# Kernel optimization log

Hardware: AMD Instinct MI355X
Metric: run time of the kernel (lower is better)

## Reference

```python
import jax, jax.numpy as jnp
import numpy as np

N = 20000        # nodes
E = 640000       # edges (avg degree 32)
D_IN = 128       # node_features
D_HID = 256      # conv_booster * D_IN
D_DENSE = 128    # D_HID // linear_decay
N_CLASSES = 2


def _glorot(key, fan_in, fan_out):
    s = np.sqrt(1.0 / fan_in).astype(np.float32)
    return jax.random.normal(key, (fan_in, fan_out), jnp.float32) * s


def setup_inputs() -> dict:
    key = jax.random.key(0)
    ks = jax.random.split(key, 12)
    return {
        "node_features": jax.random.normal(ks[0], (N, D_IN), jnp.float32),
        "edge_index": jax.random.randint(ks[1], (2, E), 0, N, dtype=jnp.int32),
        "edge_weight": jax.random.uniform(ks[2], (E,), jnp.float32),
        "W1": _glorot(ks[3], D_IN, D_HID),
        "b1": jnp.zeros((D_HID,), jnp.float32),
        "W2": _glorot(ks[4], D_HID, D_HID),
        "b2": jnp.zeros((D_HID,), jnp.float32),
        "Wd1": _glorot(ks[5], D_HID, D_DENSE),
        "bd1": jnp.zeros((D_DENSE,), jnp.float32),
        "Wd2": _glorot(ks[6], D_DENSE, N_CLASSES),
        "bd2": jnp.zeros((N_CLASSES,), jnp.float32),
    }


def gcn_conv(x, row, col, w, W, b, n):
    # PyG GCNConv: add self-loops (weight 1), symmetric normalization,
    # x' = D^{-1/2}(A+I)D^{-1/2} (x W) + b
    h = x @ W                                        # [n, out]
    loop = jnp.arange(n, dtype=row.dtype)
    r = jnp.concatenate([row, loop])
    c = jnp.concatenate([col, loop])
    ww = jnp.concatenate([w, jnp.ones((n,), w.dtype)])
    deg = jax.ops.segment_sum(ww, c, num_segments=n)  # degree at targets
    dinv = jnp.where(deg > 0, jax.lax.rsqrt(deg), 0.0)
    norm = dinv[r] * ww * dinv[c]                    # [E+n]
    msg = norm[:, None] * h[r]                       # gather + scale (hot path)
    return jax.ops.segment_sum(msg, c, num_segments=n) + b  # scatter-add


def reference(node_features, edge_index, edge_weight,
              W1, b1, W2, b2, Wd1, bd1, Wd2, bd2):
    row, col = edge_index[0], edge_index[1]
    n = node_features.shape[0]
    h = gcn_conv(node_features, row, col, edge_weight, W1, b1, n)
    h = gcn_conv(h, row, col, edge_weight, W2, b2, n)
    g = jnp.mean(h, axis=0)                          # MeanAggregation pooling
    z = jax.nn.relu(g @ Wd1 + bd1)
    logits = z @ Wd2 + bd2
    return jax.nn.softmax(logits)
```

## Files before the change

kernel.cpp:

```cpp
#include <hip/hip_runtime.h>
#include <hip/hip_bf16.h>


#define D_IN 128
#define D_HID 256
#define D_DENSE 128
#define R0 10240
#define NSL 128
#define NFOLD 250
#define FOLD_C 80
#define NTILE 157

__global__ __launch_bounds__(1024) void k_scatter(
    const int* __restrict__ tgt, const int* __restrict__ src,
    const float* __restrict__ w, const float* __restrict__ dinv,
    const float* __restrict__ u, float* __restrict__ part,
    unsigned* __restrict__ ctr, int E, int N, int mode) {
    __shared__ float acc[R0];
    if (mode == 0 && blockIdx.x == 0 && threadIdx.x == 0) ctr[0] = 0u;
    const int range = blockIdx.x & 1;
    const int slice = blockIdx.x >> 1;
    const int base  = range ? R0 : 0;
    const int lim   = range ? (N - R0) : R0;
    const int per = (E + NSL - 1) / NSL;
    const int e0 = slice * per, e1 = min(e0 + per, E);
    float* outp = part + (range ? (size_t)NSL * R0 + (size_t)slice * lim
                                : (size_t)slice * lim);
    for (int i = threadIdx.x; i < lim; i += 1024) acc[i] = 0.f;
    __syncthreads();
    for (int e = e0 + threadIdx.x; e < e1; e += 1024) {
        int t = tgt[e] - base;
        if ((unsigned)t < (unsigned)lim) {
            float v = w[e];
            if (mode != 0) {
                int c = src[e];
                float dc = dinv[c];
                v *= (mode == 2) ? dc * u[c] : dc;
            }
            atomicAdd(&acc[t], v);
        }
    }
    __syncthreads();
    for (int i = threadIdx.x; i < lim; i += 1024) outp[i] = acc[i];
}

__global__ __launch_bounds__(1024) void k_fold(
    const float* __restrict__ part, float* __restrict__ dinv,
    float* __restrict__ u, float* __restrict__ S_u_part,
    const float* __restrict__ W1, const float* __restrict__ b1,
    const float* __restrict__ W2, float* __restrict__ M, float* __restrict__ c2,
    int N, int mode) {
    __shared__ float lds[1044];
    const int b = blockIdx.x, tid = threadIdx.x;

    if (b >= NFOLD) {
        int q = b - NFOLD;
        lds[tid] = W2[(tid >> 2) * 256 + q * 4 + (tid & 3)];
        __syncthreads();
        int wvi = tid >> 6, lane = tid & 63;
        for (int kr = 0; kr < 8; ++kr) {
            int k = wvi * 8 + kr;
            float a0 = 0, a1 = 0, a2 = 0, a3 = 0;
            #pragma unroll
            for (int it = 0; it < 4; ++it) {
                int j = it * 64 + lane;
                float a = W1[k * 256 + j];
                a0 += a * lds[j*4+0]; a1 += a * lds[j*4+1];
                a2 += a * lds[j*4+2]; a3 += a * lds[j*4+3];
            }
            #pragma unroll
            for (int off = 32; off > 0; off >>= 1) {
                a0 += __shfl_down(a0, off, 64); a1 += __shfl_down(a1, off, 64);
                a2 += __shfl_down(a2, off, 64); a3 += __shfl_down(a3, off, 64);
            }
            if (lane == 0) {
                M[k * 256 + q*4 + 0] = a0; M[k * 256 + q*4 + 1] = a1;
                M[k * 256 + q*4 + 2] = a2; M[k * 256 + q*4 + 3] = a3;
            }
        }
        if (wvi == 0) {
            float a0 = 0, a1 = 0, a2 = 0, a3 = 0;
            #pragma unroll
            for (int it = 0; it < 4; ++it) {
                int j = it * 64 + lane;
                float a = b1[j];
                a0 += a * lds[j*4+0]; a1 += a * lds[j*4+1];
                a2 += a * lds[j*4+2]; a3 += a * lds[j*4+3];
            }
            #pragma unroll
            for (int off = 32; off > 0; off >>= 1) {
                a0 += __shfl_down(a0, off, 64); a1 += __shfl_down(a1, off, 64);
                a2 += __shfl_down(a2, off, 64); a3 += __shfl_down(a3, off, 64);
            }
            if (lane == 0) {
                c2[q*4+0] = a0; c2[q*4+1] = a1;
                c2[q*4+2] = a2; c2[q*4+3] = a3;
            }
        }
        return;
    }

    const int j = tid & 127, rg = tid >> 7;
    const int i = b * FOLD_C + j;
    const bool act = (j < FOLD_C) && (i < N);
    float sv = 0.f;
    if (act) {
        size_t st; const float* pp;
        if (i < R0) { st = R0;               pp = part + i; }
        else        { st = (size_t)(N - R0); pp = part + (size_t)NSL * R0 + (i - R0); }
        pp += (size_t)rg * 16 * st;
        #pragma unroll
        for (int r = 0; r < 16; ++r) sv += pp[(size_t)r * st];
    }
    lds[rg * 128 + j] = sv;
    __syncthreads();
    float ui = 0.f;
    if (rg == 0) {
        float tot = 0.f;
        #pragma unroll
        for (int q = 0; q < 8; ++q) tot += lds[q * 128 + j];
        if (act) {
            if (mode == 0) dinv[i] = rsqrtf(tot + 1.0f);
            else { float d = dinv[i]; ui = d * (tot + d); u[i] = ui; }
        }
    }
    if (mode == 1) {
        float v = ui;
        #pragma unroll
        for (int off = 32; off > 0; off >>= 1) v += __shfl_down(v, off, 64);
        if ((tid & 63) == 0) lds[1028 + (tid >> 6)] = v;
        __syncthreads();
        if (tid == 0) {
            float t2 = 0.f;
            #pragma unroll
            for (int q = 0; q < 16; ++q) t2 += lds[1028 + q];
            S_u_part[b] = t2;
        }
    }
}

__device__ __forceinline__ void g_arrive(unsigned* ctr) {
    __syncthreads();
    if (threadIdx.x == 0)
        __hip_atomic_fetch_add(ctr, 1u, __ATOMIC_RELEASE, __HIP_MEMORY_SCOPE_AGENT);
}
__device__ __forceinline__ void g_wait(unsigned* ctr, unsigned target) {
    if (threadIdx.x == 0) {
        while (__hip_atomic_load(ctr, __ATOMIC_ACQUIRE, __HIP_MEMORY_SCOPE_AGENT) < target)
            __builtin_amdgcn_s_sleep(2);
    }
    __syncthreads();
}

__global__ __launch_bounds__(1024) void k_tail(
    const float* __restrict__ x, const float* __restrict__ part,
    const float* __restrict__ dinv, const float* __restrict__ u,
    const float* __restrict__ S_u_part, const float* __restrict__ M,
    const float* __restrict__ c2, const float* __restrict__ b2,
    const float* __restrict__ Wd1, const float* __restrict__ bd1,
    const float* __restrict__ Wd2, const float* __restrict__ bd2,
    float* __restrict__ s_part, float* __restrict__ g_part,
    float* __restrict__ z_part, float* __restrict__ S_u_g,
    unsigned* __restrict__ ctr, float* __restrict__ out,
    int N, float inv_n) {
    __shared__ float sh[1024];
    __shared__ float wvl[128];
    __shared__ float ss[128];
    __shared__ float gv[16];
    __shared__ float su[16];
    const int b = blockIdx.x, tid = threadIdx.x;
    const int k = tid & 127, rg = tid >> 7;

    if (b < NTILE) {
        const int i0 = b * 128;
        const int i = i0 + k;
        const bool act = i < N;
        float sv = 0.f;
        if (act) {
            size_t st; const float* pp;
            if (i < R0) { st = R0;               pp = part + i; }
            else        { st = (size_t)(N - R0); pp = part + (size_t)NSL * R0 + (i - R0); }
            pp += (size_t)rg * 16 * st;
            #pragma unroll
            for (int r = 0; r < 16; ++r) sv += pp[(size_t)r * st];
        }
        sh[tid] = sv;
        __syncthreads();
        if (rg == 0) {
            float q = 0.f;
            #pragma unroll
            for (int t2 = 0; t2 < 8; ++t2) q += sh[t2 * 128 + k];
            float d = act ? dinv[i] : 0.f;
            wvl[k] = act ? d * (q + d * u[i]) : 0.f;
        }
        __syncthreads();
        float acc = 0.f;
        #pragma unroll
        for (int jj = 0; jj < 16; ++jj) {
            int m = rg + 8 * jj;
            int i2 = i0 + m;
            float xv = x[(size_t)(i2 < N ? i2 : i0) * D_IN + k];
            acc += wvl[m] * xv;
        }
        sh[tid] = acc;
        __syncthreads();
        if (rg == 0) {
            float t2s = 0.f;
            #pragma unroll
            for (int t2 = 0; t2 < 8; ++t2) t2s += sh[t2 * 128 + k];
            s_part[b * 128 + k] = t2s;
        }
    }
    g_arrive(ctr);
    if (b >= 16) return;
    g_wait(ctr, 256);

    {
        float a2 = 0.f;
        for (int q = rg; q < NTILE; q += 8) a2 += s_part[q * 128 + k];
        sh[tid] = a2;
        float v = 0.f;
        if (b == 0) {
            v = (tid < NFOLD) ? S_u_part[tid] : 0.f;
            #pragma unroll
            for (int off = 32; off > 0; off >>= 1) v += __shfl_down(v, off, 64);
        }
        __syncthreads();
        if (rg == 0) {
            float t2 = 0.f;
            #pragma unroll
            for (int q = 0; q < 8; ++q) t2 += sh[q * 128 + k];
            ss[k] = t2;
        }
        if (b == 0 && (tid & 63) == 0) su[tid >> 6] = v;
        __syncthreads();
        if (b == 0 && tid == 0) {
            float t2 = 0.f;
            #pragma unroll
            for (int q = 0; q < 16; ++q) t2 += su[q];
            S_u_g[0] = t2;
        }
        if (tid < 256) {
            float gp = 0.f;
            #pragma unroll
            for (int kk = 0; kk < 8; ++kk)
                gp += ss[b * 8 + kk] * M[(b * 8 + kk) * 256 + tid];
            g_part[b * 256 + tid] = gp;
        }
    }
    g_arrive(ctr);
    g_wait(ctr, 272);

    {
        if (tid < 16) {
            int kk = b * 16 + tid;
            float gval = 0.f;
            #pragma unroll
            for (int p2 = 0; p2 < 16; ++p2) gval += g_part[p2 * 256 + kk];
            gv[tid] = (gval + S_u_g[0] * c2[kk]) * inv_n + b2[kk];
        }
        __syncthreads();
        if (tid < 128) {
            float z = 0.f;
            #pragma unroll
            for (int kk = 0; kk < 16; ++kk)
                z += gv[kk] * Wd1[(b * 16 + kk) * D_DENSE + tid];
            z_part[b * 128 + tid] = z;
        }
    }
    g_arrive(ctr);
    if (b != 0) return;
    g_wait(ctr, 288);

    float p0 = 0.f, p1 = 0.f;
    if (tid < 128) {
        float zr = bd1[tid];
        #pragma unroll
        for (int p2 = 0; p2 < 16; ++p2) zr += z_part[p2 * 128 + tid];
        float zt = fmaxf(zr, 0.f);
        p0 = zt * Wd2[tid * 2 + 0];
        p1 = zt * Wd2[tid * 2 + 1];
    }
    #pragma unroll
    for (int off = 32; off > 0; off >>= 1) {
        p0 += __shfl_down(p0, off, 64);
        p1 += __shfl_down(p1, off, 64);
    }
    if ((tid & 63) == 0) { sh[tid >> 6] = p0; sh[32 + (tid >> 6)] = p1; }
    __syncthreads();
    if (tid == 0) {
        float l0 = bd2[0], l1 = bd2[1];
        #pragma unroll
        for (int q = 0; q < 16; ++q) { l0 += sh[q]; l1 += sh[32 + q]; }
        float m = fmaxf(l0, l1);
        float e0 = expf(l0 - m), e1 = expf(l1 - m);
        float inv = 1.0f / (e0 + e1);
        out[0] = e0 * inv;
        out[1] = e1 * inv;
    }
}

extern "C" void kernel_launch(void* const* d_in, const int* in_sizes, int n_in,
                              void* d_out, int out_size, void* d_ws, size_t ws_size,
                              hipStream_t stream) {
    const float* x   = (const float*)d_in[0];
    const int*   ei  = (const int*)  d_in[1];
    const float* w   = (const float*)d_in[2];
    const float* W1  = (const float*)d_in[3];
    const float* b1  = (const float*)d_in[4];
    const float* W2  = (const float*)d_in[5];
    const float* b2  = (const float*)d_in[6];
    const float* Wd1 = (const float*)d_in[7];
    const float* bd1 = (const float*)d_in[8];
    const float* Wd2 = (const float*)d_in[9];
    const float* bd2 = (const float*)d_in[10];
    float* out = (float*)d_out;

    const int N = in_sizes[0] / D_IN;
    const int E = in_sizes[1] / 2;
    const int* row = ei;
    const int* col = ei + E;

    unsigned* ctr = (unsigned*)d_ws;
    float* fws    = (float*)d_ws + 16;
    float* part   = fws;
    float* dinv   = part + (size_t)NSL * N;
    float* u      = dinv + N;
    float* s_part = u + N;
    float* S_u_p  = s_part + (size_t)NTILE * D_IN;
    float* S_u_g  = S_u_p + NFOLD;
    float* M      = S_u_g + 1;
    float* c2     = M + D_IN * D_HID;
    float* g_part = c2 + D_HID;
    float* z_part = g_part + 16 * D_HID;

    k_scatter<<<2 * NSL, 1024, 0, stream>>>(col, row, w, dinv, u, part, ctr, E, N, 0);
    k_fold<<<NFOLD + 64, 1024, 0, stream>>>(part, dinv, u, S_u_p, W1, b1, W2, M, c2, N, 0);
    k_scatter<<<2 * NSL, 1024, 0, stream>>>(row, col, w, dinv, u, part, ctr, E, N, 1);
    k_fold<<<NFOLD, 1024, 0, stream>>>(part, dinv, u, S_u_p, W1, b1, W2, M, c2, N, 1);
    k_scatter<<<2 * NSL, 1024, 0, stream>>>(row, col, w, dinv, u, part, ctr, E, N, 2);
    k_tail<<<256, 1024, 0, stream>>>(x, part, dinv, u, S_u_p, M, c2, b2,
                                     Wd1, bd1, Wd2, bd2, s_part, g_part, z_part,
                                     S_u_g, ctr, out, N, 1.0f / (float)N);
}
```

Before: 149.9 us.

## Fuse all stages into one persistent kernel with grid-wide barriers

Replaces the six separate launches (three scatters, two folds, tail) with a single 256-block persistent kernel. The stages are separated by atomic-counter grid barriers, and the counter is reset with a memset beforehand. The fold grid shrinks from 250 to 192 blocks so it fits inside the persistent grid, and the W1·W2 precompute moves onto the leftover blocks. The aim is to remove kernel launch gaps and inter-kernel drain. The cost is a spin-wait on every barrier, and the kernel relies on all 256 blocks being co-resident.

```diff
diff --git a/kernel.cpp b/kernel.cpp
--- a/kernel.cpp
+++ b/kernel.cpp
@@ -7,137 +7,9 @@
 #define D_DENSE 128
 #define R0 10240
 #define NSL 128
-#define NFOLD 250
-#define FOLD_C 80
+#define FOLD_B 192
+#define FOLD_C 105
 #define NTILE 157
-
-__global__ __launch_bounds__(1024) void k_scatter(
-    const int* __restrict__ tgt, const int* __restrict__ src,
-    const float* __restrict__ w, const float* __restrict__ dinv,
-    const float* __restrict__ u, float* __restrict__ part,
-    unsigned* __restrict__ ctr, int E, int N, int mode) {
-    __shared__ float acc[R0];
-    if (mode == 0 && blockIdx.x == 0 && threadIdx.x == 0) ctr[0] = 0u;
-    const int range = blockIdx.x & 1;
-    const int slice = blockIdx.x >> 1;
-    const int base  = range ? R0 : 0;
-    const int lim   = range ? (N - R0) : R0;
-    const int per = (E + NSL - 1) / NSL;
-    const int e0 = slice * per, e1 = min(e0 + per, E);
-    float* outp = part + (range ? (size_t)NSL * R0 + (size_t)slice * lim
-                                : (size_t)slice * lim);
-    for (int i = threadIdx.x; i < lim; i += 1024) acc[i] = 0.f;
-    __syncthreads();
-    for (int e = e0 + threadIdx.x; e < e1; e += 1024) {
-        int t = tgt[e] - base;
-        if ((unsigned)t < (unsigned)lim) {
-            float v = w[e];
-            if (mode != 0) {
-                int c = src[e];
-                float dc = dinv[c];
-                v *= (mode == 2) ? dc * u[c] : dc;
-            }
-            atomicAdd(&acc[t], v);
-        }
-    }
-    __syncthreads();
-    for (int i = threadIdx.x; i < lim; i += 1024) outp[i] = acc[i];
-}
-
-__global__ __launch_bounds__(1024) void k_fold(
-    const float* __restrict__ part, float* __restrict__ dinv,
-    float* __restrict__ u, float* __restrict__ S_u_part,
-    const float* __restrict__ W1, const float* __restrict__ b1,
-    const float* __restrict__ W2, float* __restrict__ M, float* __restrict__ c2,
-    int N, int mode) {
-    __shared__ float lds[1044];
-    const int b = blockIdx.x, tid = threadIdx.x;
-
-    if (b >= NFOLD) {
-        int q = b - NFOLD;
-        lds[tid] = W2[(tid >> 2) * 256 + q * 4 + (tid & 3)];
-        __syncthreads();
-        int wvi = tid >> 6, lane = tid & 63;
-        for (int kr = 0; kr < 8; ++kr) {
-            int k = wvi * 8 + kr;
-            float a0 = 0, a1 = 0, a2 = 0, a3 = 0;
-            #pragma unroll
-            for (int it = 0; it < 4; ++it) {
-                int j = it * 64 + lane;
-                float a = W1[k * 256 + j];
-                a0 += a * lds[j*4+0]; a1 += a * lds[j*4+1];
-                a2 += a * lds[j*4+2]; a3 += a * lds[j*4+3];
-            }
-            #pragma unroll
-            for (int off = 32; off > 0; off >>= 1) {
-                a0 += __shfl_down(a0, off, 64); a1 += __shfl_down(a1, off, 64);
-                a2 += __shfl_down(a2, off, 64); a3 += __shfl_down(a3, off, 64);
-            }
-            if (lane == 0) {
-                M[k * 256 + q*4 + 0] = a0; M[k * 256 + q*4 + 1] = a1;
-                M[k * 256 + q*4 + 2] = a2; M[k * 256 + q*4 + 3] = a3;
-            }
-        }
-        if (wvi == 0) {
-            float a0 = 0, a1 = 0, a2 = 0, a3 = 0;
-            #pragma unroll
-            for (int it = 0; it < 4; ++it) {
-                int j = it * 64 + lane;
-                float a = b1[j];
-                a0 += a * lds[j*4+0]; a1 += a * lds[j*4+1];
-                a2 += a * lds[j*4+2]; a3 += a * lds[j*4+3];
-            }
-            #pragma unroll
-            for (int off = 32; off > 0; off >>= 1) {
-                a0 += __shfl_down(a0, off, 64); a1 += __shfl_down(a1, off, 64);
-                a2 += __shfl_down(a2, off, 64); a3 += __shfl_down(a3, off, 64);
-            }
-            if (lane == 0) {
-                c2[q*4+0] = a0; c2[q*4+1] = a1;
-                c2[q*4+2] = a2; c2[q*4+3] = a3;
-            }
-        }
-        return;
-    }
-
-    const int j = tid & 127, rg = tid >> 7;
-    const int i = b * FOLD_C + j;
-    const bool act = (j < FOLD_C) && (i < N);
-    float sv = 0.f;
-    if (act) {
-        size_t st; const float* pp;
-        if (i < R0) { st = R0;               pp = part + i; }
-        else        { st = (size_t)(N - R0); pp = part + (size_t)NSL * R0 + (i - R0); }
-        pp += (size_t)rg * 16 * st;
-        #pragma unroll
-        for (int r = 0; r < 16; ++r) sv += pp[(size_t)r * st];
-    }
-    lds[rg * 128 + j] = sv;
-    __syncthreads();
-    float ui = 0.f;
-    if (rg == 0) {
-        float tot = 0.f;
-        #pragma unroll
-        for (int q = 0; q < 8; ++q) tot += lds[q * 128 + j];
-        if (act) {
-            if (mode == 0) dinv[i] = rsqrtf(tot + 1.0f);
-            else { float d = dinv[i]; ui = d * (tot + d); u[i] = ui; }
-        }
-    }
-    if (mode == 1) {
-        float v = ui;
-        #pragma unroll
-        for (int off = 32; off > 0; off >>= 1) v += __shfl_down(v, off, 64);
-        if ((tid & 63) == 0) lds[1028 + (tid >> 6)] = v;
-        __syncthreads();
-        if (tid == 0) {
-            float t2 = 0.f;
-            #pragma unroll
-            for (int q = 0; q < 16; ++q) t2 += lds[1028 + q];
-            S_u_part[b] = t2;
-        }
-    }
-}
 
 __device__ __forceinline__ void g_arrive(unsigned* ctr) {
     __syncthreads();
@@ -152,28 +24,132 @@
     __syncthreads();
 }
 
-__global__ __launch_bounds__(1024) void k_tail(
-    const float* __restrict__ x, const float* __restrict__ part,
-    const float* __restrict__ dinv, const float* __restrict__ u,
-    const float* __restrict__ S_u_part, const float* __restrict__ M,
-    const float* __restrict__ c2, const float* __restrict__ b2,
+__global__ __launch_bounds__(1024) void k_all(
+    const float* __restrict__ x, const int* __restrict__ row,
+    const int* __restrict__ col, const float* __restrict__ w,
+    const float* __restrict__ W1, const float* __restrict__ b1,
+    const float* __restrict__ W2, const float* __restrict__ b2,
     const float* __restrict__ Wd1, const float* __restrict__ bd1,
     const float* __restrict__ Wd2, const float* __restrict__ bd2,
-    float* __restrict__ s_part, float* __restrict__ g_part,
-    float* __restrict__ z_part, float* __restrict__ S_u_g,
+    float* __restrict__ part, float* __restrict__ dinv, float* __restrict__ u,
+    float* __restrict__ s_part, float* __restrict__ S_u_part,
+    float* __restrict__ S_u_g, float* __restrict__ M, float* __restrict__ c2,
+    float* __restrict__ g_part, float* __restrict__ z_part,
     unsigned* __restrict__ ctr, float* __restrict__ out,
-    int N, float inv_n) {
-    __shared__ float sh[1024];
-    __shared__ float wvl[128];
-    __shared__ float ss[128];
-    __shared__ float gv[16];
-    __shared__ float su[16];
+    int N, int E, float inv_n) {
+    __shared__ float lds[R0];
     const int b = blockIdx.x, tid = threadIdx.x;
-    const int k = tid & 127, rg = tid >> 7;
-
-    if (b < NTILE) {
-        const int i0 = b * 128;
-        const int i = i0 + k;
+
+    auto scatter = [&](const int* tgt, const int* src, int mode) {
+        const int range = b & 1, slice = b >> 1;
+        const int base = range ? R0 : 0;
+        const int lim  = range ? (N - R0) : R0;
+        const int per = (E + NSL - 1) / NSL;
+        const int e0 = slice * per, e1 = min(e0 + per, E);
+        float* outp = part + (range ? (size_t)NSL * R0 + (size_t)slice * lim
+                                    : (size_t)slice * lim);
+        for (int i = tid; i < lim; i += 1024) lds[i] = 0.f;
+        __syncthreads();
+        for (int e = e0 + tid; e < e1; e += 1024) {
+            int t = tgt[e] - base;
+            if ((unsigned)t < (unsigned)lim) {
+                float v = w[e];
+                if (mode != 0) {
+                    int c = src[e];
+                    float dc = dinv[c];
+                    v *= (mode == 2) ? dc * u[c] : dc;
+                }
+                atomicAdd(&lds[t], v);
+            }
+        }
+        __syncthreads();
+        for (int i = tid; i < lim; i += 1024) outp[i] = lds[i];
+    };
+
+    auto fold = [&](int mode) {
+        const int j = tid & 127, rg = tid >> 7;
+        const int i = b * FOLD_C + j;
+        const bool act = (j < FOLD_C) && (i < N);
+        float sv = 0.f;
+        if (act) {
+            size_t st; const float* pp;
+            if (i < R0) { st = R0;               pp = part + i; }
+            else        { st = (size_t)(N - R0); pp = part + (size_t)NSL * R0 + (i - R0); }
+            pp += (size_t)rg * 16 * st;
+            #pragma unroll
+            for (int r = 0; r < 16; ++r) sv += pp[(size_t)r * st];
+        }
+        lds[rg * 128 + j] = sv;
+        __syncthreads();
+        float ui = 0.f;
+        if (rg == 0) {
+            float tot = 0.f;
+            #pragma unroll
+            for (int q = 0; q < 8; ++q) tot += lds[q * 128 + j];
+            if (act) {
+                if (mode == 0) dinv[i] = rsqrtf(tot + 1.0f);
+                else { float d = dinv[i]; ui = d * (tot + d); u[i] = ui; }
+            }
+        }
+        if (mode == 1) {
+            float v = ui;
+            #pragma unroll
+            for (int off = 32; off > 0; off >>= 1) v += __shfl_down(v, off, 64);
+            if (tid < 128 && (tid & 63) == 0) lds[1030 + (tid >> 6)] = v;
+            __syncthreads();
+            if (tid == 0) S_u_part[b] = lds[1030] + lds[1031];
+        }
+    };
+
+    auto precompute = [&]() {
+        int q = b - FOLD_B;
+        lds[tid] = W2[(tid >> 2) * 256 + q * 4 + (tid & 3)];
+        __syncthreads();
+        int wvi = tid >> 6, lane = tid & 63;
+        for (int kr = 0; kr < 8; ++kr) {
+            int k = wvi * 8 + kr;
+            float a0 = 0, a1 = 0, a2 = 0, a3 = 0;
+            #pragma unroll
+            for (int it = 0; it < 4; ++it) {
+                int j = it * 64 + lane;
+                float a = W1[k * 256 + j];
+                a0 += a * lds[j*4+0]; a1 += a * lds[j*4+1];
+                a2 += a * lds[j*4+2]; a3 += a * lds[j*4+3];
+            }
+            #pragma unroll
+            for (int off = 32; off > 0; off >>= 1) {
+                a0 += __shfl_down(a0, off, 64); a1 += __shfl_down(a1, off, 64);
+                a2 += __shfl_down(a2, off, 64); a3 += __shfl_down(a3, off, 64);
+            }
+            if (lane == 0) {
+                M[k * 256 + q*4 + 0] = a0; M[k * 256 + q*4 + 1] = a1;
+                M[k * 256 + q*4 + 2] = a2; M[k * 256 + q*4 + 3] = a3;
+            }
+        }
+        if (wvi == 0) {
+            float a0 = 0, a1 = 0, a2 = 0, a3 = 0;
+            #pragma unroll
+            for (int it = 0; it < 4; ++it) {
+                int j = it * 64 + lane;
+                float a = b1[j];
+                a0 += a * lds[j*4+0]; a1 += a * lds[j*4+1];
+                a2 += a * lds[j*4+2]; a3 += a * lds[j*4+3];
+            }
+            #pragma unroll
+            for (int off = 32; off > 0; off >>= 1) {
+                a0 += __shfl_down(a0, off, 64); a1 += __shfl_down(a1, off, 64);
+                a2 += __shfl_down(a2, off, 64); a3 += __shfl_down(a3, off, 64);
+            }
+            if (lane == 0) {
+                c2[q*4+0] = a0; c2[q*4+1] = a1;
+                c2[q*4+2] = a2; c2[q*4+3] = a3;
+            }
+        }
+    };
+
+    auto tailA = [&]() {
+        const int k = tid & 127, rg = tid >> 7;
+        const int i0 = b * 128, i = i0 + k;
         const bool act = i < N;
         float sv = 0.f;
         if (act) {
@@ -184,14 +160,14 @@
             #pragma unroll
             for (int r = 0; r < 16; ++r) sv += pp[(size_t)r * st];
         }
-        sh[tid] = sv;
+        lds[tid] = sv;
         __syncthreads();
         if (rg == 0) {
-            float q = 0.f;
-            #pragma unroll
-            for (int t2 = 0; t2 < 8; ++t2) q += sh[t2 * 128 + k];
+            float qq = 0.f;
+            #pragma unroll
+            for (int t2 = 0; t2 < 8; ++t2) qq += lds[t2 * 128 + k];
             float d = act ? dinv[i] : 0.f;
-            wvl[k] = act ? d * (q + d * u[i]) : 0.f;
+            lds[1024 + k] = act ? d * (qq + d * u[i]) : 0.f;
         }
         __syncthreads();
         float acc = 0.f;
@@ -200,28 +176,27 @@
             int m = rg + 8 * jj;
             int i2 = i0 + m;
             float xv = x[(size_t)(i2 < N ? i2 : i0) * D_IN + k];
-            acc += wvl[m] * xv;
-        }
-        sh[tid] = acc;
+            acc += lds[1024 + m] * xv;
+        }
+        __syncthreads();
+        lds[tid] = acc;
         __syncthreads();
         if (rg == 0) {
             float t2s = 0.f;
             #pragma unroll
-            for (int t2 = 0; t2 < 8; ++t2) t2s += sh[t2 * 128 + k];
+            for (int t2 = 0; t2 < 8; ++t2) t2s += lds[t2 * 128 + k];
             s_part[b * 128 + k] = t2s;
         }
-    }
-    g_arrive(ctr);
-    if (b >= 16) return;
-    g_wait(ctr, 256);
-
-    {
+    };
+
+    auto tailB = [&]() {
+        const int k = tid & 127, rg = tid >> 7;
         float a2 = 0.f;
         for (int q = rg; q < NTILE; q += 8) a2 += s_part[q * 128 + k];
-        sh[tid] = a2;
+        lds[tid] = a2;
         float v = 0.f;
         if (b == 0) {
-            v = (tid < NFOLD) ? S_u_part[tid] : 0.f;
+            v = (tid < FOLD_B) ? S_u_part[tid] : 0.f;
             #pragma unroll
             for (int off = 32; off > 0; off >>= 1) v += __shfl_down(v, off, 64);
         }
@@ -229,75 +204,94 @@
         if (rg == 0) {
             float t2 = 0.f;
             #pragma unroll
-            for (int q = 0; q < 8; ++q) t2 += sh[q * 128 + k];
-            ss[k] = t2;
-        }
-        if (b == 0 && (tid & 63) == 0) su[tid >> 6] = v;
+            for (int q = 0; q < 8; ++q) t2 += lds[q * 128 + k];
+            lds[1024 + k] = t2;
+        }
+        if (b == 0 && (tid & 63) == 0) lds[1160 + (tid >> 6)] = v;
         __syncthreads();
         if (b == 0 && tid == 0) {
             float t2 = 0.f;
             #pragma unroll
-            for (int q = 0; q < 16; ++q) t2 += su[q];
+            for (int q = 0; q < 16; ++q) t2 += lds[1160 + q];
             S_u_g[0] = t2;
         }
         if (tid < 256) {
             float gp = 0.f;
             #pragma unroll
             for (int kk = 0; kk < 8; ++kk)
-                gp += ss[b * 8 + kk] * M[(b * 8 + kk) * 256 + tid];
+                gp += lds[1024 + b * 8 + kk] * M[(b * 8 + kk) * 256 + tid];
             g_part[b * 256 + tid] = gp;
         }
-    }
-    g_arrive(ctr);
-    g_wait(ctr, 272);
-
-    {
+    };
+
+    auto tailC = [&]() {
         if (tid < 16) {
             int kk = b * 16 + tid;
             float gval = 0.f;
             #pragma unroll
             for (int p2 = 0; p2 < 16; ++p2) gval += g_part[p2 * 256 + kk];
-            gv[tid] = (gval + S_u_g[0] * c2[kk]) * inv_n + b2[kk];
+            lds[tid] = (gval + S_u_g[0] * c2[kk]) * inv_n + b2[kk];
         }
         __syncthreads();
         if (tid < 128) {
             float z = 0.f;
             #pragma unroll
             for (int kk = 0; kk < 16; ++kk)
-                z += gv[kk] * Wd1[(b * 16 + kk) * D_DENSE + tid];
+                z += lds[kk] * Wd1[(b * 16 + kk) * D_DENSE + tid];
             z_part[b * 128 + tid] = z;
         }
-    }
+    };
+
+    auto tailD = [&]() {
+        float p0 = 0.f, p1 = 0.f;
+        if (tid < 128) {
+            float zr = bd1[tid];
+            #pragma unroll
+            for (int p2 = 0; p2 < 16; ++p2) zr += z_part[p2 * 128 + tid];
+            float zt = fmaxf(zr, 0.f);
+            p0 = zt * Wd2[tid * 2 + 0];
+            p1 = zt * Wd2[tid * 2 + 1];
+        }
+        #pragma unroll
+        for (int off = 32; off > 0; off >>= 1) {
+            p0 += __shfl_down(p0, off, 64);
+            p1 += __shfl_down(p1, off, 64);
+        }
+        if ((tid & 63) == 0) { lds[32 + (tid >> 6)] = p0; lds[64 + (tid >> 6)] = p1; }
+        __syncthreads();
+        if (tid == 0) {
+            float l0 = bd2[0], l1 = bd2[1];
+            #pragma unroll
+            for (int q = 0; q < 16; ++q) { l0 += lds[32 + q]; l1 += lds[64 + q]; }
+            float m = fmaxf(l0, l1);
+            float e0 = expf(l0 - m), e1 = expf(l1 - m);
+            float inv = 1.0f / (e0 + e1);
+            out[0] = e0 * inv;
+            out[1] = e1 * inv;
+        }
+    };
+
+    scatter(col, row, 0);
+    g_arrive(ctr); g_wait(ctr, 256);
+    if (b < FOLD_B) fold(0); else precompute();
+    g_arrive(ctr); g_wait(ctr, 512);
+    scatter(row, col, 1);
+    g_arrive(ctr); g_wait(ctr, 768);
+    if (b < FOLD_B) fold(1);
+    g_arrive(ctr); g_wait(ctr, 1024);
+    scatter(row, col, 2);
+    g_arrive(ctr); g_wait(ctr, 1280);
+    if (b < NTILE) tailA();
+    g_arrive(ctr);
+    if (b >= 16) return;
+    g_wait(ctr, 1536);
+    tailB();
+    g_arrive(ctr); g_wait(ctr, 1552);
+    tailC();
     g_arrive(ctr);
     if (b != 0) return;
-    g_wait(ctr, 288);
-
-    float p0 = 0.f, p1 = 0.f;
-    if (tid < 128) {
-        float zr = bd1[tid];
-        #pragma unroll
-        for (int p2 = 0; p2 < 16; ++p2) zr += z_part[p2 * 128 + tid];
-        float zt = fmaxf(zr, 0.f);
-        p0 = zt * Wd2[tid * 2 + 0];
-        p1 = zt * Wd2[tid * 2 + 1];
-    }
-    #pragma unroll
-    for (int off = 32; off > 0; off >>= 1) {
-        p0 += __shfl_down(p0, off, 64);
-        p1 += __shfl_down(p1, off, 64);
-    }
-    if ((tid & 63) == 0) { sh[tid >> 6] = p0; sh[32 + (tid >> 6)] = p1; }
-    __syncthreads();
-    if (tid == 0) {
-        float l0 = bd2[0], l1 = bd2[1];
-        #pragma unroll
-        for (int q = 0; q < 16; ++q) { l0 += sh[q]; l1 += sh[32 + q]; }
-        float m = fmaxf(l0, l1);
-        float e0 = expf(l0 - m), e1 = expf(l1 - m);
-        float inv = 1.0f / (e0 + e1);
-        out[0] = e0 * inv;
-        out[1] = e1 * inv;
-    }
+    g_wait(ctr, 1568);
+    tailD();
 }
 
 extern "C" void kernel_launch(void* const* d_in, const int* in_sizes, int n_in,
@@ -328,18 +322,17 @@
     float* u      = dinv + N;
     float* s_part = u + N;
     float* S_u_p  = s_part + (size_t)NTILE * D_IN;
-    float* S_u_g  = S_u_p + NFOLD;
+    float* S_u_g  = S_u_p + FOLD_B;
     float* M      = S_u_g + 1;
     float* c2     = M + D_IN * D_HID;
     float* g_part = c2 + D_HID;
     float* z_part = g_part + 16 * D_HID;
 
-    k_scatter<<<2 * NSL, 1024, 0, stream>>>(col, row, w, dinv, u, part, ctr, E, N, 0);
-    k_fold<<<NFOLD + 64, 1024, 0, stream>>>(part, dinv, u, S_u_p, W1, b1, W2, M, c2, N, 0);
-    k_scatter<<<2 * NSL, 1024, 0, stream>>>(row, col, w, dinv, u, part, ctr, E, N, 1);
-    k_fold<<<NFOLD, 1024, 0, stream>>>(part, dinv, u, S_u_p, W1, b1, W2, M, c2, N, 1);
-    k_scatter<<<2 * NSL, 1024, 0, stream>>>(row, col, w, dinv, u, part, ctr, E, N, 2);
-    k_tail<<<256, 1024, 0, stream>>>(x, part, dinv, u, S_u_p, M, c2, b2,
-                                     Wd1, bd1, Wd2, bd2, s_part, g_part, z_part,
-                                     S_u_g, ctr, out, N, 1.0f / (float)N);
+    hipMemsetAsync(ctr, 0, 64, stream);
+
+    k_all<<<256, 1024, 0, stream>>>(x, row, col, w, W1, b1, W2, b2,
+                                    Wd1, bd1, Wd2, bd2,
+                                    part, dinv, u, s_part, S_u_p, S_u_g,
+                                    M, c2, g_part, z_part, ctr, out,
+                                    N, E, 1.0f / (float)N);
 }
```

New measurement: 258.7 us. 1.73x slower.

## Replace grid-barrier tail with separate tile and single-block head kernels

Applied to the files above, without the earlier changes.

The persistent tail kernel used atomic-counter grid barriers across 256 blocks to chain the per-tile reduction, the M projection, the dense layer and the softmax. It is now split into k_tailA (157 tile blocks computing s_part) and k_head (one block doing the remaining reductions, matvecs and softmax), so kernel boundaries replace the spin barriers. The fold kernel also goes from 80 to 128 nodes per block (157 blocks instead of 250). This adds one kernel launch and serialises the small head work onto a single block, in exchange for removing the spin-wait overhead and the counter reset.

```diff
diff --git a/kernel.cpp b/kernel.cpp
--- a/kernel.cpp
+++ b/kernel.cpp
@@ -7,17 +7,14 @@
 #define D_DENSE 128
 #define R0 10240
 #define NSL 128
-#define NFOLD 250
-#define FOLD_C 80
 #define NTILE 157
 
 __global__ __launch_bounds__(1024) void k_scatter(
     const int* __restrict__ tgt, const int* __restrict__ src,
     const float* __restrict__ w, const float* __restrict__ dinv,
     const float* __restrict__ u, float* __restrict__ part,
-    unsigned* __restrict__ ctr, int E, int N, int mode) {
+    int E, int N, int mode) {
     __shared__ float acc[R0];
-    if (mode == 0 && blockIdx.x == 0 && threadIdx.x == 0) ctr[0] = 0u;
     const int range = blockIdx.x & 1;
     const int slice = blockIdx.x >> 1;
     const int base  = range ? R0 : 0;
@@ -50,11 +47,11 @@
     const float* __restrict__ W1, const float* __restrict__ b1,
     const float* __restrict__ W2, float* __restrict__ M, float* __restrict__ c2,
     int N, int mode) {
-    __shared__ float lds[1044];
+    __shared__ float lds[1056];
     const int b = blockIdx.x, tid = threadIdx.x;
 
-    if (b >= NFOLD) {
-        int q = b - NFOLD;
+    if (b >= NTILE) {
+        int q = b - NTILE;
         lds[tid] = W2[(tid >> 2) * 256 + q * 4 + (tid & 3)];
         __syncthreads();
         int wvi = tid >> 6, lane = tid & 63;
@@ -101,8 +98,8 @@
     }
 
     const int j = tid & 127, rg = tid >> 7;
-    const int i = b * FOLD_C + j;
-    const bool act = (j < FOLD_C) && (i < N);
+    const int i = b * 128 + j;
+    const bool act = i < N;
     float sv = 0.f;
     if (act) {
         size_t st; const float* pp;
@@ -128,156 +125,135 @@
         float v = ui;
         #pragma unroll
         for (int off = 32; off > 0; off >>= 1) v += __shfl_down(v, off, 64);
-        if ((tid & 63) == 0) lds[1028 + (tid >> 6)] = v;
+        if (tid < 128 && (tid & 63) == 0) lds[1028 + (tid >> 6)] = v;
         __syncthreads();
-        if (tid == 0) {
-            float t2 = 0.f;
-            #pragma unroll
-            for (int q = 0; q < 16; ++q) t2 += lds[1028 + q];
-            S_u_part[b] = t2;
-        }
-    }
-}
-
-__device__ __forceinline__ void g_arrive(unsigned* ctr) {
-    __syncthreads();
-    if (threadIdx.x == 0)
-        __hip_atomic_fetch_add(ctr, 1u, __ATOMIC_RELEASE, __HIP_MEMORY_SCOPE_AGENT);
-}
-__device__ __forceinline__ void g_wait(unsigned* ctr, unsigned target) {
-    if (threadIdx.x == 0) {
-        while (__hip_atomic_load(ctr, __ATOMIC_ACQUIRE, __HIP_MEMORY_SCOPE_AGENT) < target)
-            __builtin_amdgcn_s_sleep(2);
-    }
-    __syncthreads();
-}
-
-__global__ __launch_bounds__(1024) void k_tail(
+        if (tid == 0) S_u_part[b] = lds[1028] + lds[1029];
+    }
+}
+
+__global__ __launch_bounds__(1024) void k_tailA(
     const float* __restrict__ x, const float* __restrict__ part,
     const float* __restrict__ dinv, const float* __restrict__ u,
-    const float* __restrict__ S_u_part, const float* __restrict__ M,
-    const float* __restrict__ c2, const float* __restrict__ b2,
-    const float* __restrict__ Wd1, const float* __restrict__ bd1,
-    const float* __restrict__ Wd2, const float* __restrict__ bd2,
-    float* __restrict__ s_part, float* __restrict__ g_part,
-    float* __restrict__ z_part, float* __restrict__ S_u_g,
-    unsigned* __restrict__ ctr, float* __restrict__ out,
-    int N, float inv_n) {
+    float* __restrict__ s_part, int N) {
     __shared__ float sh[1024];
     __shared__ float wvl[128];
-    __shared__ float ss[128];
-    __shared__ float gv[16];
-    __shared__ float su[16];
     const int b = blockIdx.x, tid = threadIdx.x;
     const int k = tid & 127, rg = tid >> 7;
-
-    if (b < NTILE) {
-        const int i0 = b * 128;
-        const int i = i0 + k;
-        const bool act = i < N;
-        float sv = 0.f;
-        if (act) {
-            size_t st; const float* pp;
-            if (i < R0) { st = R0;               pp = part + i; }
-            else        { st = (size_t)(N - R0); pp = part + (size_t)NSL * R0 + (i - R0); }
-            pp += (size_t)rg * 16 * st;
-            #pragma unroll
-            for (int r = 0; r < 16; ++r) sv += pp[(size_t)r * st];
-        }
-        sh[tid] = sv;
+    const int i0 = b * 128, i = i0 + k;
+    const bool act = i < N;
+    float sv = 0.f;
+    if (act) {
+        size_t st; const float* pp;
+        if (i < R0) { st = R0;               pp = part + i; }
+        else        { st = (size_t)(N - R0); pp = part + (size_t)NSL * R0 + (i - R0); }
+        pp += (size_t)rg * 16 * st;
+        #pragma unroll
+        for (int r = 0; r < 16; ++r) sv += pp[(size_t)r * st];
+    }
+    sh[tid] = sv;
+    __syncthreads();
+    if (rg == 0) {
+        float q = 0.f;
+        #pragma unroll
+        for (int t2 = 0; t2 < 8; ++t2) q += sh[t2 * 128 + k];
+        float d = act ? dinv[i] : 0.f;
+        wvl[k] = act ? d * (q + d * u[i]) : 0.f;
+    }
+    __syncthreads();
+    float acc = 0.f;
+    #pragma unroll
+    for (int jj = 0; jj < 16; ++jj) {
+        int m = rg + 8 * jj;
+        int i2 = i0 + m;
+        float xv = x[(size_t)(i2 < N ? i2 : i0) * D_IN + k];
+        acc += wvl[m] * xv;
+    }
+    __syncthreads();
+    sh[tid] = acc;
+    __syncthreads();
+    if (rg == 0) {
+        float t2s = 0.f;
+        #pragma unroll
+        for (int t2 = 0; t2 < 8; ++t2) t2s += sh[t2 * 128 + k];
+        s_part[b * 128 + k] = t2s;
+    }
+}
+
+__global__ __launch_bounds__(1024) void k_head(
+    const float* __restrict__ s_part, const float* __restrict__ S_u_part,
+    const float* __restrict__ M, const float* __restrict__ c2,
+    const float* __restrict__ b2, const float* __restrict__ Wd1,
+    const float* __restrict__ bd1, const float* __restrict__ Wd2,
+    const float* __restrict__ bd2, float* __restrict__ out, float inv_n) {
+    __shared__ float sh[1024];
+    __shared__ float ss[128];
+    __shared__ float gg[256];
+    __shared__ float zz[128];
+    __shared__ float red[40];
+    const int tid = threadIdx.x;
+    const int k = tid & 127, rg = tid >> 7;
+
+    float a = 0.f;
+    for (int q = rg; q < NTILE; q += 8) a += s_part[q * 128 + k];
+    sh[tid] = a;
+    float v = (tid < NTILE) ? S_u_part[tid] : 0.f;
+    #pragma unroll
+    for (int off = 32; off > 0; off >>= 1) v += __shfl_down(v, off, 64);
+    __syncthreads();
+    if (rg == 0) {
+        float t2 = 0.f;
+        #pragma unroll
+        for (int q = 0; q < 8; ++q) t2 += sh[q * 128 + k];
+        ss[k] = t2;
+    }
+    if ((tid & 63) == 0) red[tid >> 6] = v;
+    __syncthreads();
+    if (tid == 0) {
+        float t2 = 0.f;
+        #pragma unroll
+        for (int q = 0; q < 16; ++q) t2 += red[q];
+        red[16] = t2;
+    }
+    __syncthreads();
+    const float S_u = red[16];
+
+    {
+        int t = tid & 255, kg = tid >> 8;
+        float acc = 0.f;
+        #pragma unroll
+        for (int kk = 0; kk < 32; ++kk) {
+            int k2 = kg * 32 + kk;
+            acc += ss[k2] * M[k2 * 256 + t];
+        }
+        sh[tid] = acc;
         __syncthreads();
-        if (rg == 0) {
-            float q = 0.f;
-            #pragma unroll
-            for (int t2 = 0; t2 < 8; ++t2) q += sh[t2 * 128 + k];
-            float d = act ? dinv[i] : 0.f;
-            wvl[k] = act ? d * (q + d * u[i]) : 0.f;
-        }
-        __syncthreads();
+        if (kg == 0)
+            gg[t] = (sh[t] + sh[256 + t] + sh[512 + t] + sh[768 + t]
+                     + S_u * c2[t]) * inv_n + b2[t];
+    }
+    __syncthreads();
+
+    {
         float acc = 0.f;
         #pragma unroll
-        for (int jj = 0; jj < 16; ++jj) {
-            int m = rg + 8 * jj;
-            int i2 = i0 + m;
-            float xv = x[(size_t)(i2 < N ? i2 : i0) * D_IN + k];
-            acc += wvl[m] * xv;
+        for (int kk = 0; kk < 32; ++kk) {
+            int k2 = rg * 32 + kk;
+            acc += gg[k2] * Wd1[k2 * D_DENSE + k];
         }
         sh[tid] = acc;
         __syncthreads();
         if (rg == 0) {
-            float t2s = 0.f;
-            #pragma unroll
-            for (int t2 = 0; t2 < 8; ++t2) t2s += sh[t2 * 128 + k];
-            s_part[b * 128 + k] = t2s;
-        }
-    }
-    g_arrive(ctr);
-    if (b >= 16) return;
-    g_wait(ctr, 256);
-
-    {
-        float a2 = 0.f;
-        for (int q = rg; q < NTILE; q += 8) a2 += s_part[q * 128 + k];
-        sh[tid] = a2;
-        float v = 0.f;
-        if (b == 0) {
-            v = (tid < NFOLD) ? S_u_part[tid] : 0.f;
-            #pragma unroll
-            for (int off = 32; off > 0; off >>= 1) v += __shfl_down(v, off, 64);
-        }
-        __syncthreads();
-        if (rg == 0) {
-            float t2 = 0.f;
-            #pragma unroll
-            for (int q = 0; q < 8; ++q) t2 += sh[q * 128 + k];
-            ss[k] = t2;
-        }
-        if (b == 0 && (tid & 63) == 0) su[tid >> 6] = v;
-        __syncthreads();
-        if (b == 0 && tid == 0) {
-            float t2 = 0.f;
-            #pragma unroll
-            for (int q = 0; q < 16; ++q) t2 += su[q];
-            S_u_g[0] = t2;
-        }
-        if (tid < 256) {
-            float gp = 0.f;
-            #pragma unroll
-            for (int kk = 0; kk < 8; ++kk)
-                gp += ss[b * 8 + kk] * M[(b * 8 + kk) * 256 + tid];
-            g_part[b * 256 + tid] = gp;
-        }
-    }
-    g_arrive(ctr);
-    g_wait(ctr, 272);
-
-    {
-        if (tid < 16) {
-            int kk = b * 16 + tid;
-            float gval = 0.f;
-            #pragma unroll
-            for (int p2 = 0; p2 < 16; ++p2) gval += g_part[p2 * 256 + kk];
-            gv[tid] = (gval + S_u_g[0] * c2[kk]) * inv_n + b2[kk];
-        }
-        __syncthreads();
-        if (tid < 128) {
             float z = 0.f;
             #pragma unroll
-            for (int kk = 0; kk < 16; ++kk)
-                z += gv[kk] * Wd1[(b * 16 + kk) * D_DENSE + tid];
-            z_part[b * 128 + tid] = z;
-        }
-    }
-    g_arrive(ctr);
-    if (b != 0) return;
-    g_wait(ctr, 288);
+            for (int q = 0; q < 8; ++q) z += sh[q * 128 + k];
+            zz[k] = fmaxf(z + bd1[k], 0.f);
+        }
+    }
+    __syncthreads();
 
     float p0 = 0.f, p1 = 0.f;
     if (tid < 128) {
-        float zr = bd1[tid];
-        #pragma unroll
-        for (int p2 = 0; p2 < 16; ++p2) zr += z_part[p2 * 128 + tid];
-        float zt = fmaxf(zr, 0.f);
+        float zt = zz[tid];
         p0 = zt * Wd2[tid * 2 + 0];
         p1 = zt * Wd2[tid * 2 + 1];
     }
@@ -286,12 +262,11 @@
         p0 += __shfl_down(p0, off, 64);
         p1 += __shfl_down(p1, off, 64);
     }
-    if ((tid & 63) == 0) { sh[tid >> 6] = p0; sh[32 + (tid >> 6)] = p1; }
+    if ((tid & 63) == 0) { red[tid >> 6] = p0; red[20 + (tid >> 6)] = p1; }
     __syncthreads();
     if (tid == 0) {
-        float l0 = bd2[0], l1 = bd2[1];
-        #pragma unroll
-        for (int q = 0; q < 16; ++q) { l0 += sh[q]; l1 += sh[32 + q]; }
+        float l0 = red[0] + red[1] + bd2[0];
+        float l1 = red[20] + red[21] + bd2[1];
         float m = fmaxf(l0, l1);
         float e0 = expf(l0 - m), e1 = expf(l1 - m);
         float inv = 1.0f / (e0 + e1);
@@ -321,25 +296,21 @@
     const int* row = ei;
     const int* col = ei + E;
 
-    unsigned* ctr = (unsigned*)d_ws;
-    float* fws    = (float*)d_ws + 16;
+    float* fws    = (float*)d_ws;
     float* part   = fws;
     float* dinv   = part + (size_t)NSL * N;
     float* u      = dinv + N;
     float* s_part = u + N;
     float* S_u_p  = s_part + (size_t)NTILE * D_IN;
-    float* S_u_g  = S_u_p + NFOLD;
-    float* M      = S_u_g + 1;
+    float* M      = S_u_p + NTILE;
     float* c2     = M + D_IN * D_HID;
-    float* g_part = c2 + D_HID;
-    float* z_part = g_part + 16 * D_HID;
-
-    k_scatter<<<2 * NSL, 1024, 0, stream>>>(col, row, w, dinv, u, part, ctr, E, N, 0);
-    k_fold<<<NFOLD + 64, 1024, 0, stream>>>(part, dinv, u, S_u_p, W1, b1, W2, M, c2, N, 0);
-    k_scatter<<<2 * NSL, 1024, 0, stream>>>(row, col, w, dinv, u, part, ctr, E, N, 1);
-    k_fold<<<NFOLD, 1024, 0, stream>>>(part, dinv, u, S_u_p, W1, b1, W2, M, c2, N, 1);
-    k_scatter<<<2 * NSL, 1024, 0, stream>>>(row, col, w, dinv, u, part, ctr, E, N, 2);
-    k_tail<<<256, 1024, 0, stream>>>(x, part, dinv, u, S_u_p, M, c2, b2,
-                                     Wd1, bd1, Wd2, bd2, s_part, g_part, z_part,
-                                     S_u_g, ctr, out, N, 1.0f / (float)N);
-}
+
+    k_scatter<<<2 * NSL, 1024, 0, stream>>>(col, row, w, dinv, u, part, E, N, 0);
+    k_fold<<<NTILE + 64, 1024, 0, stream>>>(part, dinv, u, S_u_p, W1, b1, W2, M, c2, N, 0);
+    k_scatter<<<2 * NSL, 1024, 0, stream>>>(row, col, w, dinv, u, part, E, N, 1);
+    k_fold<<<NTILE, 1024, 0, stream>>>(part, dinv, u, S_u_p, W1, b1, W2, M, c2, N, 1);
+    k_scatter<<<2 * NSL, 1024, 0, stream>>>(row, col, w, dinv, u, part, E, N, 2);
+    k_tailA<<<NTILE, 1024, 0, stream>>>(x, part, dinv, u, s_part, N);
+    k_head<<<1, 1024, 0, stream>>>(s_part, S_u_p, M, c2, b2, Wd1, bd1, Wd2, bd2,
+                                   out, 1.0f / (float)N);
+}
```

Result: no change. 152.1 us (+1.5%).
